# Performance work log

Measured on AMD Instinct MI355X. Metric: run time of the kernel, lower is better.

The kernel has to match this reference:

```python
import jax, jax.numpy as jnp
import numpy as np

IMAGE_MAX_DIM = 1024
POOL = 7
NUM_CLASSES = 81
N_ROIS = 2000
BN_EPS = 1e-3


def _make_boxes(key, n):
    k1, k2, k3, k4 = jax.random.split(key, 4)
    cx = jax.random.uniform(k1, (n,), minval=0.0, maxval=IMAGE_MAX_DIM)
    cy = jax.random.uniform(k2, (n,), minval=0.0, maxval=IMAGE_MAX_DIM)
    w = jax.random.uniform(k3, (n,), minval=16.0, maxval=512.0)
    h = jax.random.uniform(k4, (n,), minval=16.0, maxval=512.0)
    x1 = jnp.clip(cx - w / 2, 0.0, IMAGE_MAX_DIM - 2.0)
    y1 = jnp.clip(cy - h / 2, 0.0, IMAGE_MAX_DIM - 2.0)
    x2 = jnp.clip(cx + w / 2, x1 + 1.0, IMAGE_MAX_DIM)
    y2 = jnp.clip(cy + h / 2, y1 + 1.0, IMAGE_MAX_DIM)
    return jnp.stack([x1, y1, x2, y2], axis=-1)[None]  # [1, n, 4]


def setup_inputs() -> dict:
    key = jax.random.key(0)
    ks = jax.random.split(key, 16)
    d = {
        'p2': jax.random.normal(ks[0], (1, 256, 256, 256), jnp.float32),
        'p3': jax.random.normal(ks[1], (1, 256, 128, 128), jnp.float32),
        'p4': jax.random.normal(ks[2], (1, 256, 64, 64), jnp.float32),
        'p5': jax.random.normal(ks[3], (1, 256, 32, 32), jnp.float32),
        'rpn_rois': _make_boxes(ks[4], N_ROIS),
        'conv1_w': jax.random.normal(ks[5], (1024, 256, POOL, POOL), jnp.float32) * 0.02,
        'conv1_b': jnp.zeros((1024,), jnp.float32),
        'bn1_g': jnp.ones((1024,), jnp.float32),
        'bn1_b': jnp.zeros((1024,), jnp.float32),
        'bn1_m': jnp.zeros((1024,), jnp.float32),
        'bn1_v': jnp.ones((1024,), jnp.float32),
        'conv2_w': jax.random.normal(ks[6], (1024, 1024), jnp.float32) * 0.02,
        'conv2_b': jnp.zeros((1024,), jnp.float32),
        'bn2_g': jnp.ones((1024,), jnp.float32),
        'bn2_b': jnp.zeros((1024,), jnp.float32),
        'bn2_m': jnp.zeros((1024,), jnp.float32),
        'bn2_v': jnp.ones((1024,), jnp.float32),
        'logits_w': jax.random.normal(ks[7], (NUM_CLASSES, 1024), jnp.float32) * 0.02,
        'logits_b': jnp.zeros((NUM_CLASSES,), jnp.float32),
        'bbox_w': jax.random.normal(ks[8], (NUM_CLASSES * 4, 1024), jnp.float32) * 0.02,
        'bbox_b': jnp.zeros((NUM_CLASSES * 4,), jnp.float32),
    }
    return d


def _crop_resize(fmap, boxes):
    """TF-style crop_and_resize, bilinear. fmap [C,H,W]; boxes [N,4] = (y1,x1,y2,x2) normalized."""
    C, H, W = fmap.shape
    dt = fmap.dtype
    y1, x1, y2, x2 = boxes[:, 0], boxes[:, 1], boxes[:, 2], boxes[:, 3]
    t = (jnp.arange(POOL, dtype=dt) / (POOL - 1))  # [P]
    ys = y1[:, None] * (H - 1) + t[None, :] * ((y2 - y1) * (H - 1))[:, None]  # [N,P]
    xs = x1[:, None] * (W - 1) + t[None, :] * ((x2 - x1) * (W - 1))[:, None]  # [N,P]
    y0 = jnp.floor(ys)
    x0 = jnp.floor(xs)
    ly = (ys - y0)[None, :, :, None]  # [1,N,P,1]
    lx = (xs - x0)[None, :, None, :]  # [1,N,1,P]
    y0i = jnp.clip(y0.astype(jnp.int32), 0, H - 1)
    y1i = jnp.clip(y0i + 1, 0, H - 1)
    x0i = jnp.clip(x0.astype(jnp.int32), 0, W - 1)
    x1i = jnp.clip(x0i + 1, 0, W - 1)

    def g(yi, xi):  # -> [C,N,P,P]
        return fmap[:, yi[:, :, None], xi[:, None, :]]

    out = (g(y0i, x0i) * (1 - ly) * (1 - lx) + g(y0i, x1i) * (1 - ly) * lx
           + g(y1i, x0i) * ly * (1 - lx) + g(y1i, x1i) * ly * lx)
    return jnp.transpose(out, (1, 0, 2, 3))  # [N,C,P,P]


def _forward(p2, p3, p4, p5, rpn_rois, conv1_w, conv1_b, bn1_g, bn1_b, bn1_m, bn1_v,
             conv2_w, conv2_b, bn2_g, bn2_b, bn2_m, bn2_v, logits_w, logits_b, bbox_w, bbox_b):
    rois = rpn_rois.reshape(-1, 4)  # [N,4] (x1,y1,x2,y2) in pixels
    x1, y1, x2, y2 = rois[:, 0], rois[:, 1], rois[:, 2], rois[:, 3]
    # level = clamp(round(log2(sqrt(area)/224)) + 4, 2, 5)
    roi_level = jnp.clip(jnp.round(jnp.log2(jnp.sqrt((y2 - y1) * (x2 - x1)) / 224.0)) + 4.0, 2.0, 5.0)
    boxes_n = (rois / float(IMAGE_MAX_DIM))[:, [1, 0, 3, 2]]  # (y1,x1,y2,x2) normalized

    pooled = jnp.zeros((rois.shape[0], 256, POOL, POOL), rois.dtype)
    for lvl, fmap in zip(range(2, 6), [p2, p3, p4, p5]):
        crops = _crop_resize(fmap[0], boxes_n)  # [N,256,P,P]
        mask = (roi_level == float(lvl))[:, None, None, None]
        pooled = pooled + jnp.where(mask, crops, 0.0)

    # conv1: 7x7 valid conv over [N,256,7,7] -> [N,1024]
    h = jnp.einsum('nchw,ochw->no', pooled, conv1_w) + conv1_b
    h = (h - bn1_m) * jax.lax.rsqrt(bn1_v + BN_EPS) * bn1_g + bn1_b
    h = jax.nn.relu(h)
    # conv2: 1x1 conv == matmul
    h = h @ conv2_w.T + conv2_b
    h = (h - bn2_m) * jax.lax.rsqrt(bn2_v + BN_EPS) * bn2_g + bn2_b
    shared = jax.nn.relu(h)  # [N,1024]

    logits = shared @ logits_w.T + logits_b
    probs = jax.nn.softmax(logits, axis=-1)
    bbox = shared @ bbox_w.T + bbox_b
    return (logits.reshape(1, N_ROIS, NUM_CLASSES),
            probs.reshape(1, N_ROIS, NUM_CLASSES),
            bbox.reshape(1, N_ROIS, NUM_CLASSES, 4))


def reference(p2, p3, p4, p5, rpn_rois, conv1_w, conv1_b, bn1_g, bn1_b, bn1_m, bn1_v,
              conv2_w, conv2_b, bn2_g, bn2_b, bn2_m, bn2_v, logits_w, logits_b, bbox_w, bbox_b):
    return _forward(p2, p3, p4, p5, rpn_rois, conv1_w, conv1_b, bn1_g, bn1_b, bn1_m, bn1_v,
                    conv2_w, conv2_b, bn2_g, bn2_b, bn2_m, bn2_v, logits_w, logits_b, bbox_w, bbox_b)
```

## Files before the change

### kernel.cpp

```cpp
#include <hip/hip_runtime.h>
#include <stdint.h>

#define NROI 2000
#define MPAD 2048
#define KP   12544
#define N1   1024
#define NCLS 81
#define NBOX 324
#define N3   405
#define N3P  448
#define BN_EPS 0.001f
#define KSPLIT 8
#define KC    1568

typedef __attribute__((ext_vector_type(8))) short bf16x8;
typedef __attribute__((ext_vector_type(4))) float f32x4;

__device__ inline unsigned short f2bf(float f) {
  union { float f; unsigned u; } v; v.f = f;
  unsigned r = v.u + 0x7fffu + ((v.u >> 16) & 1u);
  return (unsigned short)(r >> 16);
}

__device__ inline float bf2f(unsigned short h) {
  union { unsigned u; float f; } v; v.u = (unsigned)h << 16; return v.f;
}

__device__ inline void gld16(const unsigned short* g, unsigned short* l) {
  __builtin_amdgcn_global_load_lds(
      (const __attribute__((address_space(1))) void*)g,
      (__attribute__((address_space(3))) void*)l, 16, 0, 0);
}

__global__ __launch_bounds__(256) void prep_all(
    const float* __restrict__ c1w, const float* __restrict__ c2w,
    const float* __restrict__ lw, const float* __restrict__ bw,
    const float* c1b, const float* g1, const float* b1, const float* m1, const float* v1,
    const float* c2b, const float* g2, const float* b2, const float* m2, const float* v2,
    const float* lb, const float* bb,
    unsigned short* __restrict__ w1p, unsigned short* __restrict__ w2b,
    unsigned short* __restrict__ w3b,
    float* s1, float* t1, float* s2, float* t2, float* b3) {
  __shared__ unsigned short s[KP];
  int b = blockIdx.x;
  int t = threadIdx.x;
  if (b < 1024) {
    const float* src = c1w + (size_t)b * KP;
    for (int j = t; j < KP; j += 256) s[j] = f2bf(src[j]);
    __syncthreads();
    unsigned short* dst = w1p + (size_t)b * KP;
    int lane = t & 63, w = t >> 6;
    int c4 = lane * 4;
    for (int j = w; j < 49; j += 4) {
      ushort4 o;
      o.x = s[(c4 + 0) * 49 + j];
      o.y = s[(c4 + 1) * 49 + j];
      o.z = s[(c4 + 2) * 49 + j];
      o.w = s[(c4 + 3) * 49 + j];
      *(ushort4*)(dst + j * 256 + c4) = o;
    }
  } else if (b < 5120) {
    int j = (b - 1024) * 256 + t;
    w2b[j] = f2bf(c2w[j]);
  } else if (b < 5568) {
    int row = b - 5120;
    for (int k = t; k < 1024; k += 256) {
      float v = (row < NCLS) ? lw[row * 1024 + k]
                             : (row < N3 ? bw[(row - NCLS) * 1024 + k] : 0.0f);
      w3b[row * 1024 + k] = f2bf(v);
    }
  } else {
    for (int i = t; i < 1024; i += 256) {
      float sc = g1[i] * rsqrtf(v1[i] + BN_EPS);
      s1[i] = sc;
      t1[i] = (c1b[i] - m1[i]) * sc + b1[i];
      float ss = g2[i] * rsqrtf(v2[i] + BN_EPS);
      s2[i] = ss;
      t2[i] = (c2b[i] - m2[i]) * ss + b2[i];
    }
    for (int i = t; i < N3P; i += 256)
      b3[i] = (i < NCLS) ? lb[i] : (i < N3 ? bb[i - NCLS] : 0.0f);
  }
}

__global__ __launch_bounds__(256) void transpose_all(
    const float* __restrict__ p2, const float* __restrict__ p3,
    const float* __restrict__ p4, const float* __restrict__ p5,
    unsigned short* __restrict__ f2t, unsigned short* __restrict__ f3t,
    unsigned short* __restrict__ f4t, unsigned short* __restrict__ f5t) {
  __shared__ unsigned short s[64][260];
  int b = blockIdx.x;
  const float* src;
  unsigned short* dst;
  int HW;
  if (b < 1024)      { src = p2; dst = f2t; HW = 65536; }
  else if (b < 1280) { b -= 1024; src = p3; dst = f3t; HW = 16384; }
  else if (b < 1344) { b -= 1280; src = p4; dst = f4t; HW = 4096; }
  else               { b -= 1344; src = p5; dst = f5t; HW = 1024; }
  int p0 = b * 64;
  int t = threadIdx.x;
  int lane = t & 63, w = t >> 6;
  int px0 = (lane & 15) * 4;
#pragma unroll 4
  for (int it = 0; it < 16; ++it) {
    int c = w * 64 + it * 4 + (lane >> 4);
    float4 v = *(const float4*)(src + (size_t)c * HW + p0 + px0);
    s[px0 + 0][c] = f2bf(v.x);
    s[px0 + 1][c] = f2bf(v.y);
    s[px0 + 2][c] = f2bf(v.z);
    s[px0 + 3][c] = f2bf(v.w);
  }
  __syncthreads();
  int c4 = lane * 4;
#pragma unroll 4
  for (int i = 0; i < 16; ++i) {
    int p = w * 16 + i;
    ushort4 o = *(const ushort4*)&s[p][c4];
    *(ushort4*)(dst + (size_t)(p0 + p) * 256 + c4) = o;
  }
}

__global__ __launch_bounds__(256) void roi_align2(
    const unsigned short* __restrict__ f2t, const unsigned short* __restrict__ f3t,
    const unsigned short* __restrict__ f4t, const unsigned short* __restrict__ f5t,
    const float* __restrict__ rois, unsigned short* __restrict__ pooled) {
  int n = blockIdx.x;
  int t = threadIdx.x;
  int lane = t & 63, w = t >> 6;
  int c0 = lane * 4;
  unsigned short* out = pooled + (size_t)n * KP;
  if (n >= NROI) {
    for (int p = w; p < 49; p += 4)
      *(ushort4*)(out + p * 256 + c0) = make_ushort4(0, 0, 0, 0);
    return;
  }
  float x1 = rois[n * 4 + 0], y1 = rois[n * 4 + 1];
  float x2 = rois[n * 4 + 2], y2 = rois[n * 4 + 3];
  float area = (y2 - y1) * (x2 - x1);
  float lvl_f = rintf(log2f(sqrtf(area) / 224.0f)) + 4.0f;
  lvl_f = fminf(fmaxf(lvl_f, 2.0f), 5.0f);
  int lvl = (int)lvl_f;
  const unsigned short* f;
  int H;
  if (lvl == 2)      { f = f2t; H = 256; }
  else if (lvl == 3) { f = f3t; H = 128; }
  else if (lvl == 4) { f = f4t; H = 64;  }
  else               { f = f5t; H = 32;  }
  int W = H;
  const float inv = 1.0f / 1024.0f;
  float yn1 = y1 * inv, xn1 = x1 * inv, yn2 = y2 * inv, xn2 = x2 * inv;
  float hs = (yn2 - yn1) * (H - 1);
  float ws = (xn2 - xn1) * (W - 1);
  float yb = yn1 * (H - 1);
  float xb = xn1 * (W - 1);

  for (int p = w; p < 49; p += 4) {
    int py = p / 7, px = p - py * 7;
    float ysv = yb + ((float)py / 6.0f) * hs;
    float xsv = xb + ((float)px / 6.0f) * ws;
    float y0f = floorf(ysv), x0f = floorf(xsv);
    float ly = ysv - y0f, lx = xsv - x0f;
    int y0 = min(max((int)y0f, 0), H - 1);
    int y1i = min(y0 + 1, H - 1);
    int x0 = min(max((int)x0f, 0), W - 1);
    int x1i = min(x0 + 1, W - 1);
    ushort4 v00 = *(const ushort4*)(f + ((size_t)y0 * W + x0) * 256 + c0);
    ushort4 v01 = *(const ushort4*)(f + ((size_t)y0 * W + x1i) * 256 + c0);
    ushort4 v10 = *(const ushort4*)(f + ((size_t)y1i * W + x0) * 256 + c0);
    ushort4 v11 = *(const ushort4*)(f + ((size_t)y1i * W + x1i) * 256 + c0);
    ushort4 o;
    {
      float a = bf2f(v00.x), bq = bf2f(v01.x), cq = bf2f(v10.x), d = bf2f(v11.x);
      float top = a + lx * (bq - a), bot = cq + lx * (d - cq);
      o.x = f2bf(top + ly * (bot - top));
    }
    {
      float a = bf2f(v00.y), bq = bf2f(v01.y), cq = bf2f(v10.y), d = bf2f(v11.y);
      float top = a + lx * (bq - a), bot = cq + lx * (d - cq);
      o.y = f2bf(top + ly * (bot - top));
    }
    {
      float a = bf2f(v00.z), bq = bf2f(v01.z), cq = bf2f(v10.z), d = bf2f(v11.z);
      float top = a + lx * (bq - a), bot = cq + lx * (d - cq);
      o.z = f2bf(top + ly * (bot - top));
    }
    {
      float a = bf2f(v00.w), bq = bf2f(v01.w), cq = bf2f(v10.w), d = bf2f(v11.w);
      float top = a + lx * (bq - a), bot = cq + lx * (d - cq);
      o.w = f2bf(top + ly * (bot - top));
    }
    *(ushort4*)(out + p * 256 + c0) = o;
  }
}

__global__ __launch_bounds__(256) void gemm1_sk(
    const unsigned short* __restrict__ A, const unsigned short* __restrict__ B,
    float* __restrict__ part) {
  __shared__ unsigned short As[128 * 64];
  __shared__ unsigned short Bs[128 * 64];
  int bid = blockIdx.x;
  int kz = bid & 7;
  int u = bid >> 3;
  int bn0 = (u & 7) * 128;
  int bm0 = (u >> 3) * 128;
  int t = threadIdx.x;
  int lane = t & 63, w = t >> 6;
  int wm = (w & 1) * 64, wn = (w >> 1) * 64;
  int ln = lane & 15, q = lane >> 4;

  int r8 = t >> 3, j8 = t & 7;
  int sj = j8 ^ (r8 & 7);
  const unsigned short* ga = A + (size_t)(bm0 + r8) * KP + kz * KC + sj * 8;
  const unsigned short* gb = B + (size_t)(bn0 + r8) * KP + kz * KC + sj * 8;
  unsigned short* la = &As[t * 8];
  unsigned short* lb = &Bs[t * 8];
  int e = ln & 7;

  f32x4 acc[4][4] = {};

  for (int k0 = 0; k0 < 1536; k0 += 64) {
#pragma unroll
    for (int i = 0; i < 4; ++i) {
      gld16(ga + k0 + (size_t)(i * 32) * KP, la + i * 2048);
      gld16(gb + k0 + (size_t)(i * 32) * KP, lb + i * 2048);
    }
    __syncthreads();
#pragma unroll
    for (int h = 0; h < 2; ++h) {
      int slot = ((h * 4 + q) ^ e) * 8;
      bf16x8 af[4], bfr[4];
#pragma unroll
      for (int i = 0; i < 4; ++i) {
        af[i]  = *(const bf16x8*)&As[(wm + i * 16 + ln) * 64 + slot];
        bfr[i] = *(const bf16x8*)&Bs[(wn + i * 16 + ln) * 64 + slot];
      }
#pragma unroll
      for (int i = 0; i < 4; ++i)
#pragma unroll
        for (int j = 0; j < 4; ++j)
          acc[i][j] = __builtin_amdgcn_mfma_f32_16x16x32_bf16(af[i], bfr[j], acc[i][j], 0, 0, 0);
    }
    __syncthreads();
  }
  {
    const unsigned short* ga2 = A + (size_t)(bm0 + (t >> 2)) * KP + kz * KC + 1536 + (t & 3) * 8;
    const unsigned short* gb2 = B + (size_t)(bn0 + (t >> 2)) * KP + kz * KC + 1536 + (t & 3) * 8;
    gld16(ga2, &As[t * 8]);
    gld16(ga2 + (size_t)64 * KP, &As[t * 8 + 2048]);
    gld16(gb2, &Bs[t * 8]);
    gld16(gb2 + (size_t)64 * KP, &Bs[t * 8 + 2048]);
    __syncthreads();
    bf16x8 af[4], bfr[4];
#pragma unroll
    for (int i = 0; i < 4; ++i) {
      af[i]  = *(const bf16x8*)&As[(wm + i * 16 + ln) * 32 + q * 8];
      bfr[i] = *(const bf16x8*)&Bs[(wn + i * 16 + ln) * 32 + q * 8];
    }
#pragma unroll
    for (int i = 0; i < 4; ++i)
#pragma unroll
      for (int j = 0; j < 4; ++j)
        acc[i][j] = __builtin_amdgcn_mfma_f32_16x16x32_bf16(af[i], bfr[j], acc[i][j], 0, 0, 0);
  }

  float* po = part + (size_t)kz * MPAD * N1;
#pragma unroll
  for (int i = 0; i < 4; ++i)
#pragma unroll
    for (int j = 0; j < 4; ++j)
#pragma unroll
      for (int r = 0; r < 4; ++r) {
        int m = bm0 + wm + i * 16 + q * 4 + r;
        int n = bn0 + wn + j * 16 + ln;
        po[(size_t)m * N1 + n] = acc[i][j][r];
      }
}

__global__ void reduce_sk(const float* __restrict__ part,
                          const float* __restrict__ sc, const float* __restrict__ sh,
                          unsigned short* __restrict__ outb) {
  const size_t P = (size_t)MPAD * N1;
  int m = blockIdx.x;
  int t = threadIdx.x;
  float4 v = {0.f, 0.f, 0.f, 0.f};
#pragma unroll
  for (int kz = 0; kz < KSPLIT; ++kz) {
    const float4* pk = (const float4*)(part + kz * P + (size_t)m * N1);
    float4 u = pk[t];
    v.x += u.x; v.y += u.y; v.z += u.z; v.w += u.w;
  }
  int n0 = t * 4;
  ushort4 o;
  if (m < NROI) {
    o.x = f2bf(fmaxf(v.x * sc[n0 + 0] + sh[n0 + 0], 0.0f));
    o.y = f2bf(fmaxf(v.y * sc[n0 + 1] + sh[n0 + 1], 0.0f));
    o.z = f2bf(fmaxf(v.z * sc[n0 + 2] + sh[n0 + 2], 0.0f));
    o.w = f2bf(fmaxf(v.w * sc[n0 + 3] + sh[n0 + 3], 0.0f));
  } else {
    o = make_ushort4(0, 0, 0, 0);
  }
  *(ushort4*)(outb + (size_t)m * N1 + n0) = o;
}

template <int MODE>
__global__ __launch_bounds__(256) void gemm_bt(
    const unsigned short* __restrict__ A, const unsigned short* __restrict__ B,
    int M, int N, int K,
    const float* __restrict__ sc, const float* __restrict__ sh,
    unsigned short* __restrict__ outb, float* __restrict__ outf,
    int validM, int ldo) {
  __shared__ unsigned short As[64 * 64];
  __shared__ unsigned short Bs[64 * 64];
  int bm0 = blockIdx.y * 64;
  int bn0 = blockIdx.x * 64;
  int t = threadIdx.x;
  int lane = t & 63, w = t >> 6;
  int wm = (w & 1) * 32, wn = (w >> 1) * 32;
  int ln = lane & 15, q = lane >> 4;

  int r8 = t >> 3, j8 = t & 7;
  int sj = j8 ^ (r8 & 7);
  const unsigned short* ga = A + (size_t)(bm0 + r8) * K + sj * 8;
  const unsigned short* gb = B + (size_t)(bn0 + r8) * K + sj * 8;
  unsigned short* la = &As[t * 8];
  unsigned short* lb = &Bs[t * 8];
  int e = ln & 7;

  f32x4 acc00 = {0.f, 0.f, 0.f, 0.f}, acc01 = {0.f, 0.f, 0.f, 0.f};
  f32x4 acc10 = {0.f, 0.f, 0.f, 0.f}, acc11 = {0.f, 0.f, 0.f, 0.f};

  for (int k0 = 0; k0 < K; k0 += 64) {
    gld16(ga + k0, la);
    gld16(ga + k0 + (size_t)32 * K, la + 2048);
    gld16(gb + k0, lb);
    gld16(gb + k0 + (size_t)32 * K, lb + 2048);
    __syncthreads();
#pragma unroll
    for (int h = 0; h < 2; ++h) {
      int slot = ((h * 4 + q) ^ e) * 8;
      bf16x8 a0 = *(const bf16x8*)&As[(wm + ln) * 64 + slot];
      bf16x8 a1 = *(const bf16x8*)&As[(wm + 16 + ln) * 64 + slot];
      bf16x8 b0 = *(const bf16x8*)&Bs[(wn + ln) * 64 + slot];
      bf16x8 b1 = *(const bf16x8*)&Bs[(wn + 16 + ln) * 64 + slot];
      acc00 = __builtin_amdgcn_mfma_f32_16x16x32_bf16(a0, b0, acc00, 0, 0, 0);
      acc01 = __builtin_amdgcn_mfma_f32_16x16x32_bf16(a0, b1, acc01, 0, 0, 0);
      acc10 = __builtin_amdgcn_mfma_f32_16x16x32_bf16(a1, b0, acc10, 0, 0, 0);
      acc11 = __builtin_amdgcn_mfma_f32_16x16x32_bf16(a1, b1, acc11, 0, 0, 0);
    }
    __syncthreads();
  }

  f32x4 accs[2][2] = {{acc00, acc01}, {acc10, acc11}};
#pragma unroll
  for (int i = 0; i < 2; ++i)
#pragma unroll
    for (int j = 0; j < 2; ++j)
#pragma unroll
      for (int r = 0; r < 4; ++r) {
        int m = bm0 + wm + i * 16 + q * 4 + r;
        int n = bn0 + wn + j * 16 + ln;
        float v = accs[i][j][r];
        if (MODE == 1) {
          float o = fmaxf(v * sc[n] + sh[n], 0.0f);
          outb[(size_t)m * ldo + n] = (m < validM) ? f2bf(o) : (unsigned short)0;
        } else {
          outf[(size_t)m * ldo + n] = v + sh[n];
        }
      }
}

__global__ void head(const float* __restrict__ fc3, float* __restrict__ out) {
  int r = blockIdx.x;
  int t = threadIdx.x;
  const float* row = fc3 + (size_t)r * N3P;
  float v0 = (t < NCLS) ? row[t] : -INFINITY;
  float v1 = (t + 64 < NCLS) ? row[t + 64] : -INFINITY;
  float m = fmaxf(v0, v1);
#pragma unroll
  for (int o = 32; o > 0; o >>= 1) m = fmaxf(m, __shfl_xor(m, o, 64));
  float e0 = (t < NCLS) ? expf(v0 - m) : 0.0f;
  float e1 = (t + 64 < NCLS) ? expf(v1 - m) : 0.0f;
  float s = e0 + e1;
#pragma unroll
  for (int o = 32; o > 0; o >>= 1) s += __shfl_xor(s, o, 64);
  float invs = 1.0f / s;
  float* ol = out + (size_t)r * NCLS;
  float* op = out + 162000 + (size_t)r * NCLS;
  float* ob = out + 324000 + (size_t)r * NBOX;
  if (t < NCLS) { ol[t] = v0; op[t] = e0 * invs; }
  if (t + 64 < NCLS) { ol[t + 64] = v1; op[t + 64] = e1 * invs; }
  for (int j = t; j < NBOX; j += 64) ob[j] = row[NCLS + j];
}

extern "C" void kernel_launch(void* const* d_in, const int* in_sizes, int n_in,
                              void* d_out, int out_size, void* d_ws, size_t ws_size,
                              hipStream_t stream) {
  const float* p2  = (const float*)d_in[0];
  const float* p3  = (const float*)d_in[1];
  const float* p4  = (const float*)d_in[2];
  const float* p5  = (const float*)d_in[3];
  const float* roi = (const float*)d_in[4];
  const float* c1w = (const float*)d_in[5];
  const float* c1b = (const float*)d_in[6];
  const float* g1  = (const float*)d_in[7];
  const float* b1  = (const float*)d_in[8];
  const float* m1  = (const float*)d_in[9];
  const float* v1  = (const float*)d_in[10];
  const float* c2w = (const float*)d_in[11];
  const float* c2b = (const float*)d_in[12];
  const float* g2  = (const float*)d_in[13];
  const float* b2  = (const float*)d_in[14];
  const float* m2  = (const float*)d_in[15];
  const float* v2  = (const float*)d_in[16];
  const float* lw  = (const float*)d_in[17];
  const float* lb  = (const float*)d_in[18];
  const float* bw  = (const float*)d_in[19];
  const float* bb  = (const float*)d_in[20];
  float* out = (float*)d_out;

  char* ws = (char*)d_ws;
  size_t off = 0;
  auto alloc = [&](size_t bytes) {
    void* p = ws + off;
    off = (off + bytes + 255) & ~(size_t)255;
    return p;
  };
  unsigned short* pooled = (unsigned short*)alloc((size_t)MPAD * KP * 2);
  unsigned short* w1p    = (unsigned short*)alloc((size_t)N1 * KP * 2);
  unsigned short* w2b    = (unsigned short*)alloc((size_t)N1 * N1 * 2);
  unsigned short* w3b    = (unsigned short*)alloc((size_t)N3P * N1 * 2);
  unsigned short* a2     = (unsigned short*)alloc((size_t)MPAD * N1 * 2);
  unsigned short* shd    = (unsigned short*)alloc((size_t)MPAD * N1 * 2);
  float* fc3 = (float*)alloc((size_t)MPAD * N3P * 4);
  char* ub = (char*)alloc((size_t)KSPLIT * MPAD * N1 * 4);
  unsigned short* f2t = (unsigned short*)ub;
  unsigned short* f3t = (unsigned short*)(ub + 33554432);
  unsigned short* f4t = (unsigned short*)(ub + 33554432 + 8388608);
  unsigned short* f5t = (unsigned short*)(ub + 33554432 + 8388608 + 2097152);
  float* part = (float*)ub;
  float* s1  = (float*)alloc(1024 * 4);
  float* t1  = (float*)alloc(1024 * 4);
  float* s2  = (float*)alloc(1024 * 4);
  float* t2  = (float*)alloc(1024 * 4);
  float* b3  = (float*)alloc(N3P * 4);

  prep_all<<<5569, 256, 0, stream>>>(c1w, c2w, lw, bw,
                                     c1b, g1, b1, m1, v1, c2b, g2, b2, m2, v2,
                                     lb, bb, w1p, w2b, w3b, s1, t1, s2, t2, b3);

  transpose_all<<<1360, 256, 0, stream>>>(p2, p3, p4, p5, f2t, f3t, f4t, f5t);

  roi_align2<<<MPAD, 256, 0, stream>>>(f2t, f3t, f4t, f5t, roi, pooled);

  gemm1_sk<<<1024, 256, 0, stream>>>(pooled, w1p, part);
  reduce_sk<<<MPAD, 256, 0, stream>>>(part, s1, t1, a2);

  gemm_bt<1><<<dim3(N1 / 64, MPAD / 64), 256, 0, stream>>>(
      a2, w2b, MPAD, N1, N1, s2, t2, shd, nullptr, NROI, N1);
  gemm_bt<2><<<dim3(N3P / 64, MPAD / 64), 256, 0, stream>>>(
      shd, w3b, MPAD, N3P, N1, nullptr, b3, nullptr, fc3, NROI, N3P);

  head<<<NROI, 64, 0, stream>>>(fc3, out);
}
```

Before: 352.8 us.

## Merge prep and transpose kernels, store split-K partials as bf16, simplify K slicing

Combines the weight-prep and feature-transpose kernels into one launch with shared LDS storage. This removes one kernel boundary and lets the two independent jobs overlap. Split-K partial sums are now stored as bf16 instead of fp32, halving the partial-buffer write and read traffic between gemm1 and the reduction, at some cost in accumulation precision. The K split now uses uneven slices that are all multiples of 64, which removes the tail iteration.

```diff
diff --git a/kernel.cpp b/kernel.cpp
--- a/kernel.cpp
+++ b/kernel.cpp
@@ -11,7 +11,6 @@
 #define N3P  448
 #define BN_EPS 0.001f
 #define KSPLIT 8
-#define KC    1568
 
 typedef __attribute__((ext_vector_type(8))) short bf16x8;
 typedef __attribute__((ext_vector_type(4))) float f32x4;
@@ -32,19 +31,29 @@
       (__attribute__((address_space(3))) void*)l, 16, 0, 0);
 }
 
-__global__ __launch_bounds__(256) void prep_all(
+__device__ __forceinline__ void kslice(int kz, int& off, int& len) {
+  if (kz < 4) { off = kz * 1536; len = 1536; }
+  else        { off = 6144 + (kz - 4) * 1600; len = 1600; }
+}
+
+__global__ __launch_bounds__(256) void front(
     const float* __restrict__ c1w, const float* __restrict__ c2w,
     const float* __restrict__ lw, const float* __restrict__ bw,
     const float* c1b, const float* g1, const float* b1, const float* m1, const float* v1,
     const float* c2b, const float* g2, const float* b2, const float* m2, const float* v2,
     const float* lb, const float* bb,
+    const float* __restrict__ p2, const float* __restrict__ p3,
+    const float* __restrict__ p4, const float* __restrict__ p5,
     unsigned short* __restrict__ w1p, unsigned short* __restrict__ w2b,
     unsigned short* __restrict__ w3b,
+    unsigned short* __restrict__ f2t, unsigned short* __restrict__ f3t,
+    unsigned short* __restrict__ f4t, unsigned short* __restrict__ f5t,
     float* s1, float* t1, float* s2, float* t2, float* b3) {
-  __shared__ unsigned short s[KP];
+  __shared__ char smem_raw[64 * 260 * 2];
   int b = blockIdx.x;
   int t = threadIdx.x;
   if (b < 1024) {
+    unsigned short* s = (unsigned short*)smem_raw;
     const float* src = c1w + (size_t)b * KP;
     for (int j = t; j < KP; j += 256) s[j] = f2bf(src[j]);
     __syncthreads();
@@ -69,7 +78,7 @@
                              : (row < N3 ? bw[(row - NCLS) * 1024 + k] : 0.0f);
       w3b[row * 1024 + k] = f2bf(v);
     }
-  } else {
+  } else if (b == 5568) {
     for (int i = t; i < 1024; i += 256) {
       float sc = g1[i] * rsqrtf(v1[i] + BN_EPS);
       s1[i] = sc;
@@ -80,43 +89,37 @@
     }
     for (int i = t; i < N3P; i += 256)
       b3[i] = (i < NCLS) ? lb[i] : (i < N3 ? bb[i - NCLS] : 0.0f);
-  }
-}
-
-__global__ __launch_bounds__(256) void transpose_all(
-    const float* __restrict__ p2, const float* __restrict__ p3,
-    const float* __restrict__ p4, const float* __restrict__ p5,
-    unsigned short* __restrict__ f2t, unsigned short* __restrict__ f3t,
-    unsigned short* __restrict__ f4t, unsigned short* __restrict__ f5t) {
-  __shared__ unsigned short s[64][260];
-  int b = blockIdx.x;
-  const float* src;
-  unsigned short* dst;
-  int HW;
-  if (b < 1024)      { src = p2; dst = f2t; HW = 65536; }
-  else if (b < 1280) { b -= 1024; src = p3; dst = f3t; HW = 16384; }
-  else if (b < 1344) { b -= 1280; src = p4; dst = f4t; HW = 4096; }
-  else               { b -= 1344; src = p5; dst = f5t; HW = 1024; }
-  int p0 = b * 64;
-  int t = threadIdx.x;
-  int lane = t & 63, w = t >> 6;
-  int px0 = (lane & 15) * 4;
+  } else {
+    typedef unsigned short lds_t[64][260];
+    lds_t& s = *(lds_t*)smem_raw;
+    int bb2 = b - 5569;
+    const float* src;
+    unsigned short* dst;
+    int HW;
+    if (bb2 < 1024)      { src = p2; dst = f2t; HW = 65536; }
+    else if (bb2 < 1280) { bb2 -= 1024; src = p3; dst = f3t; HW = 16384; }
+    else if (bb2 < 1344) { bb2 -= 1280; src = p4; dst = f4t; HW = 4096; }
+    else                 { bb2 -= 1344; src = p5; dst = f5t; HW = 1024; }
+    int p0 = bb2 * 64;
+    int lane = t & 63, w = t >> 6;
+    int px0 = (lane & 15) * 4;
 #pragma unroll 4
-  for (int it = 0; it < 16; ++it) {
-    int c = w * 64 + it * 4 + (lane >> 4);
-    float4 v = *(const float4*)(src + (size_t)c * HW + p0 + px0);
-    s[px0 + 0][c] = f2bf(v.x);
-    s[px0 + 1][c] = f2bf(v.y);
-    s[px0 + 2][c] = f2bf(v.z);
-    s[px0 + 3][c] = f2bf(v.w);
-  }
-  __syncthreads();
-  int c4 = lane * 4;
+    for (int it = 0; it < 16; ++it) {
+      int c = w * 64 + it * 4 + (lane >> 4);
+      float4 v = *(const float4*)(src + (size_t)c * HW + p0 + px0);
+      s[px0 + 0][c] = f2bf(v.x);
+      s[px0 + 1][c] = f2bf(v.y);
+      s[px0 + 2][c] = f2bf(v.z);
+      s[px0 + 3][c] = f2bf(v.w);
+    }
+    __syncthreads();
+    int c4 = lane * 4;
 #pragma unroll 4
-  for (int i = 0; i < 16; ++i) {
-    int p = w * 16 + i;
-    ushort4 o = *(const ushort4*)&s[p][c4];
-    *(ushort4*)(dst + (size_t)(p0 + p) * 256 + c4) = o;
+    for (int i = 0; i < 16; ++i) {
+      int p = w * 16 + i;
+      ushort4 o = *(const ushort4*)&s[p][c4];
+      *(ushort4*)(dst + (size_t)(p0 + p) * 256 + c4) = o;
+    }
   }
 }
 
@@ -195,7 +198,7 @@
 
 __global__ __launch_bounds__(256) void gemm1_sk(
     const unsigned short* __restrict__ A, const unsigned short* __restrict__ B,
-    float* __restrict__ part) {
+    unsigned short* __restrict__ part) {
   __shared__ unsigned short As[128 * 64];
   __shared__ unsigned short Bs[128 * 64];
   int bid = blockIdx.x;
@@ -203,6 +206,8 @@
   int u = bid >> 3;
   int bn0 = (u & 7) * 128;
   int bm0 = (u >> 3) * 128;
+  int koff, klen;
+  kslice(kz, koff, klen);
   int t = threadIdx.x;
   int lane = t & 63, w = t >> 6;
   int wm = (w & 1) * 64, wn = (w >> 1) * 64;
@@ -210,15 +215,15 @@
 
   int r8 = t >> 3, j8 = t & 7;
   int sj = j8 ^ (r8 & 7);
-  const unsigned short* ga = A + (size_t)(bm0 + r8) * KP + kz * KC + sj * 8;
-  const unsigned short* gb = B + (size_t)(bn0 + r8) * KP + kz * KC + sj * 8;
+  const unsigned short* ga = A + (size_t)(bm0 + r8) * KP + koff + sj * 8;
+  const unsigned short* gb = B + (size_t)(bn0 + r8) * KP + koff + sj * 8;
   unsigned short* la = &As[t * 8];
   unsigned short* lb = &Bs[t * 8];
   int e = ln & 7;
 
   f32x4 acc[4][4] = {};
 
-  for (int k0 = 0; k0 < 1536; k0 += 64) {
+  for (int k0 = 0; k0 < klen; k0 += 64) {
 #pragma unroll
     for (int i = 0; i < 4; ++i) {
       gld16(ga + k0 + (size_t)(i * 32) * KP, la + i * 2048);
@@ -242,28 +247,8 @@
     }
     __syncthreads();
   }
-  {
-    const unsigned short* ga2 = A + (size_t)(bm0 + (t >> 2)) * KP + kz * KC + 1536 + (t & 3) * 8;
-    const unsigned short* gb2 = B + (size_t)(bn0 + (t >> 2)) * KP + kz * KC + 1536 + (t & 3) * 8;
-    gld16(ga2, &As[t * 8]);
-    gld16(ga2 + (size_t)64 * KP, &As[t * 8 + 2048]);
-    gld16(gb2, &Bs[t * 8]);
-    gld16(gb2 + (size_t)64 * KP, &Bs[t * 8 + 2048]);
-    __syncthreads();
-    bf16x8 af[4], bfr[4];
-#pragma unroll
-    for (int i = 0; i < 4; ++i) {
-      af[i]  = *(const bf16x8*)&As[(wm + i * 16 + ln) * 32 + q * 8];
-      bfr[i] = *(const bf16x8*)&Bs[(wn + i * 16 + ln) * 32 + q * 8];
-    }
-#pragma unroll
-    for (int i = 0; i < 4; ++i)
-#pragma unroll
-      for (int j = 0; j < 4; ++j)
-        acc[i][j] = __builtin_amdgcn_mfma_f32_16x16x32_bf16(af[i], bfr[j], acc[i][j], 0, 0, 0);
-  }
-
-  float* po = part + (size_t)kz * MPAD * N1;
+
+  unsigned short* po = part + (size_t)kz * MPAD * N1;
 #pragma unroll
   for (int i = 0; i < 4; ++i)
 #pragma unroll
@@ -272,11 +257,11 @@
       for (int r = 0; r < 4; ++r) {
         int m = bm0 + wm + i * 16 + q * 4 + r;
         int n = bn0 + wn + j * 16 + ln;
-        po[(size_t)m * N1 + n] = acc[i][j][r];
+        po[(size_t)m * N1 + n] = f2bf(acc[i][j][r]);
       }
 }
 
-__global__ void reduce_sk(const float* __restrict__ part,
+__global__ void reduce_sk(const unsigned short* __restrict__ part,
                           const float* __restrict__ sc, const float* __restrict__ sh,
                           unsigned short* __restrict__ outb) {
   const size_t P = (size_t)MPAD * N1;
@@ -285,9 +270,8 @@
   float4 v = {0.f, 0.f, 0.f, 0.f};
 #pragma unroll
   for (int kz = 0; kz < KSPLIT; ++kz) {
-    const float4* pk = (const float4*)(part + kz * P + (size_t)m * N1);
-    float4 u = pk[t];
-    v.x += u.x; v.y += u.y; v.z += u.z; v.w += u.w;
+    ushort4 u = *(const ushort4*)(part + kz * P + (size_t)m * N1 + t * 4);
+    v.x += bf2f(u.x); v.y += bf2f(u.y); v.z += bf2f(u.z); v.w += bf2f(u.w);
   }
   int n0 = t * 4;
   ushort4 o;
@@ -432,23 +416,23 @@
   unsigned short* a2     = (unsigned short*)alloc((size_t)MPAD * N1 * 2);
   unsigned short* shd    = (unsigned short*)alloc((size_t)MPAD * N1 * 2);
   float* fc3 = (float*)alloc((size_t)MPAD * N3P * 4);
-  char* ub = (char*)alloc((size_t)KSPLIT * MPAD * N1 * 4);
+  char* ub = (char*)alloc((size_t)48 * 1024 * 1024);
   unsigned short* f2t = (unsigned short*)ub;
   unsigned short* f3t = (unsigned short*)(ub + 33554432);
   unsigned short* f4t = (unsigned short*)(ub + 33554432 + 8388608);
   unsigned short* f5t = (unsigned short*)(ub + 33554432 + 8388608 + 2097152);
-  float* part = (float*)ub;
+  unsigned short* part = (unsigned short*)ub;
   float* s1  = (float*)alloc(1024 * 4);
   float* t1  = (float*)alloc(1024 * 4);
   float* s2  = (float*)alloc(1024 * 4);
   float* t2  = (float*)alloc(1024 * 4);
   float* b3  = (float*)alloc(N3P * 4);
 
-  prep_all<<<5569, 256, 0, stream>>>(c1w, c2w, lw, bw,
-                                     c1b, g1, b1, m1, v1, c2b, g2, b2, m2, v2,
-                                     lb, bb, w1p, w2b, w3b, s1, t1, s2, t2, b3);
-
-  transpose_all<<<1360, 256, 0, stream>>>(p2, p3, p4, p5, f2t, f3t, f4t, f5t);
+  front<<<6929, 256, 0, stream>>>(c1w, c2w, lw, bw,
+                                  c1b, g1, b1, m1, v1, c2b, g2, b2, m2, v2,
+                                  lb, bb, p2, p3, p4, p5,
+                                  w1p, w2b, w3b, f2t, f3t, f4t, f5t,
+                                  s1, t1, s2, t2, b3);
 
   roi_align2<<<MPAD, 256, 0, stream>>>(f2t, f3t, f4t, f5t, roi, pooled);
 
```

After: 330.7 us. -6.3%, faster.
